# Optimization experiments

Measured on AMD Instinct MI355X. Metric: run time of the kernel, lower is better.

## Reference

```python
import jax, jax.numpy as jnp
import numpy as np

N, IN_DIM, H1, H2, LIN, MAX_INDEX = 16384, 64, 256, 256, 64, 256


def _init_layer(key, out_dim, in_dim):
    # mimic kaiming_uniform(a=sqrt(5)) + uniform bias bound = 1/sqrt(fan_in)
    kW, kb = jax.random.split(key)
    bound_w = 1.0 / np.sqrt(in_dim)  # gain*sqrt(3/fan_in) with a=sqrt(5) -> 1/sqrt(fan_in)
    W = jax.random.uniform(kW, (MAX_INDEX, out_dim, in_dim), jnp.float32, -bound_w, bound_w)
    b = jax.random.uniform(kb, (MAX_INDEX, out_dim), jnp.float32, -bound_w, bound_w)
    return W, b


def setup_inputs() -> dict:
    key = jax.random.key(0)
    kx, ki, k1, k2, k3 = jax.random.split(key, 5)
    x = jax.random.normal(kx, (N, IN_DIM), jnp.float32)
    ind = jax.random.randint(ki, (N,), 0, MAX_INDEX, jnp.int64 if jax.config.jax_enable_x64 else jnp.int32)
    W1, b1 = _init_layer(k1, H1, IN_DIM)
    W2, b2 = _init_layer(k2, H2, H1)
    Wl, bl = _init_layer(k3, LIN, H2)
    return {"x": x, "ind": ind, "W1": W1, "b1": b1, "W2": W2, "b2": b2, "Wl": Wl, "bl": bl}


def _index_linear(x, ind, W, b):
    # per-row expert weight gather then row-wise matvec: out[n] = W[ind[n]] @ x[n] + b[ind[n]]
    return jnp.einsum('noi,ni->no', W[ind], x) + b[ind]


def reference(x, ind, W1, b1, W2, b2, Wl, bl):
    h = jnp.tanh(_index_linear(x, ind, W1, b1))
    h = jnp.tanh(_index_linear(h, ind, W2, b2))
    return _index_linear(h, ind, Wl, bl)
```

## Files before the change

kernel.cpp:

```cpp
#include <hip/hip_runtime.h>
#include <hip/hip_bf16.h>
#include <math.h>

#define NROWS   16384
#define IN_DIM  64
#define HID     256
#define OUT_DIM 64
#define NEXP    256
#define MT      32
#define HP      264

typedef __attribute__((ext_vector_type(8))) short short8;
typedef __attribute__((ext_vector_type(4))) float f32x4;
typedef __attribute__((ext_vector_type(4))) unsigned uint4v;
typedef __attribute__((ext_vector_type(2))) unsigned uint2v;


__global__ __launch_bounds__(1024) void prep_k(const int* __restrict__ ind,
                                               int* __restrict__ rows,
                                               int* __restrict__ offsets) {
  __shared__ int hist[NEXP];
  __shared__ int scan[NEXP];
  __shared__ int cur[NEXP];
  int t = threadIdx.x;
  if (t < NEXP) hist[t] = 0;
  __syncthreads();
  for (int n = t; n < NROWS; n += 1024) atomicAdd(&hist[ind[n]], 1);
  __syncthreads();
  if (t < NEXP) scan[t] = hist[t];
  __syncthreads();
  for (int d = 1; d < NEXP; d <<= 1) {
    int v = (t < NEXP && t >= d) ? scan[t - d] : 0;
    __syncthreads();
    if (t < NEXP) scan[t] += v;
    __syncthreads();
  }
  if (t < NEXP) {
    int exc = scan[t] - hist[t];
    offsets[t] = exc;
    cur[t] = exc;
    if (t == NEXP - 1) offsets[NEXP] = scan[t];
  }
  __syncthreads();
  for (int n = t; n < NROWS; n += 1024) {
    int p = atomicAdd(&cur[ind[n]], 1);
    rows[p] = n;
  }
}


__device__ __forceinline__ unsigned pk2_trunc(float a, float b) {
  unsigned ua = __builtin_bit_cast(unsigned, a);
  unsigned ub = __builtin_bit_cast(unsigned, b);
  return (ub & 0xffff0000u) | (ua >> 16);
}

__device__ __forceinline__ unsigned pk2_rn(float a, float b) {
  __hip_bfloat162 h = __float22bfloat162_rn(float2{a, b});
  unsigned r;
  __builtin_memcpy(&r, &h, 4);
  return r;
}

__device__ __forceinline__ short8 cvt8w(f32x4 w0, f32x4 w1) {
  uint4v u;
  u.x = pk2_trunc(w0.x, w0.y);
  u.y = pk2_trunc(w0.z, w0.w);
  u.z = pk2_trunc(w1.x, w1.y);
  u.w = pk2_trunc(w1.z, w1.w);
  return __builtin_bit_cast(short8, u);
}

__device__ __forceinline__ float fast_tanh(float v) {
  float e = __expf(2.f * v);
  return 1.f - 2.f * __builtin_amdgcn_rcpf(e + 1.f);
}

template <int K, int NMT, int NNT>
__device__ __forceinline__ void layer_mm(const float* __restrict__ Wp,
                                         const float* __restrict__ bp,
                                         const unsigned short* Hin,
                                         int l15, int q, f32x4 (&acc)[NMT][NNT]) {
#pragma unroll
  for (int mt = 0; mt < NMT; mt++) {
    f32x4 bv = *(const f32x4*)(bp + mt * 16 + q * 4);
#pragma unroll
    for (int nt = 0; nt < NNT; nt++) acc[mt][nt] = bv;
  }
  const float* wr[NMT];
#pragma unroll
  for (int mt = 0; mt < NMT; mt++)
    wr[mt] = Wp + (size_t)(mt * 16 + l15) * K + q * 8;

  constexpr int KS = K / 32;
  f32x4 wcur[NMT][2], wnxt[NMT][2];
#pragma unroll
  for (int mt = 0; mt < NMT; mt++) {
    wcur[mt][0] = *(const f32x4*)(wr[mt]);
    wcur[mt][1] = *(const f32x4*)(wr[mt] + 4);
  }
#pragma unroll
  for (int ks = 0; ks < KS; ks++) {
    int kn = (ks + 1 < KS) ? (ks + 1) * 32 : 0;
#pragma unroll
    for (int mt = 0; mt < NMT; mt++) {
      wnxt[mt][0] = *(const f32x4*)(wr[mt] + kn);
      wnxt[mt][1] = *(const f32x4*)(wr[mt] + kn + 4);
    }
    short8 bfr[NNT];
#pragma unroll
    for (int nt = 0; nt < NNT; nt++)
      bfr[nt] = *(const short8*)&Hin[(nt * 16 + l15) * HP + ks * 32 + q * 8];
#pragma unroll
    for (int mt = 0; mt < NMT; mt++) {
      short8 a = cvt8w(wcur[mt][0], wcur[mt][1]);
#pragma unroll
      for (int nt = 0; nt < NNT; nt++)
        acc[mt][nt] =
            __builtin_amdgcn_mfma_f32_16x16x32_bf16(a, bfr[nt], acc[mt][nt], 0, 0, 0);
    }
#pragma unroll
    for (int mt = 0; mt < NMT; mt++) {
      wcur[mt][0] = wnxt[mt][0];
      wcur[mt][1] = wnxt[mt][1];
    }
  }
}

template <int NNT>
__device__ __forceinline__ void write_h(f32x4 (&acc)[4][NNT], unsigned short* H,
                                        int w, int l15, int q) {
#pragma unroll
  for (int mt = 0; mt < 4; mt++)
#pragma unroll
    for (int nt = 0; nt < NNT; nt++) {
      uint2v v;
      v.x = pk2_rn(fast_tanh(acc[mt][nt].x), fast_tanh(acc[mt][nt].y));
      v.y = pk2_rn(fast_tanh(acc[mt][nt].z), fast_tanh(acc[mt][nt].w));
      *(uint2v*)&H[(nt * 16 + l15) * HP + w * 64 + mt * 16 + q * 4] = v;
    }
}


__global__ __launch_bounds__(256, 2) void mlp_k(
    const float* __restrict__ x,
    const float* __restrict__ W1, const float* __restrict__ b1,
    const float* __restrict__ W2, const float* __restrict__ b2,
    const float* __restrict__ Wl, const float* __restrict__ bl,
    const int* __restrict__ rows, const int* __restrict__ offsets,
    float* __restrict__ out) {
  __shared__ __align__(16) unsigned short H[MT * HP];

  const int t = threadIdx.x;
  const int w = t >> 6;
  const int l15 = t & 15;
  const int q = (t >> 4) & 3;
  const int e = blockIdx.x & 255;
  const int j = blockIdx.x >> 8;
  const int beg = offsets[e];
  const int cnt = offsets[e + 1] - beg;

  const float* W1e = W1 + (size_t)e * HID * IN_DIM + (size_t)(w * 64) * IN_DIM;
  const float* W2e = W2 + (size_t)e * HID * HID + (size_t)(w * 64) * HID;
  const float* Wle = Wl + (size_t)e * OUT_DIM * HID + (size_t)(w * 16) * HID;
  const float* b1e = b1 + e * HID + w * 64;
  const float* b2e = b2 + e * HID + w * 64;
  const float* ble = bl + e * OUT_DIM + w * 16;

  const int sm = t >> 3;
  const int sc = (t & 7) * 8;

  for (int mt0 = j * MT; mt0 < cnt; mt0 += 2 * MT) {
    __syncthreads();
    {
      int gm = mt0 + sm;
      bool val = gm < cnt;
      int r = val ? rows[beg + gm] : 0;
      const float* xr = x + (size_t)r * IN_DIM + sc;
      uint4v u;
      if (val) {
        f32x4 a0 = *(const f32x4*)(xr);
        f32x4 a1 = *(const f32x4*)(xr + 4);
        u.x = pk2_rn(a0.x, a0.y); u.y = pk2_rn(a0.z, a0.w);
        u.z = pk2_rn(a1.x, a1.y); u.w = pk2_rn(a1.z, a1.w);
      } else {
        u = (uint4v){0, 0, 0, 0};
      }
      *(uint4v*)&H[sm * HP + sc] = u;
    }
    __syncthreads();

    {
      f32x4 acc[4][2];
      layer_mm<IN_DIM, 4, 2>(W1e, b1e, H, l15, q, acc);
      __syncthreads();
      write_h<2>(acc, H, w, l15, q);
    }
    __syncthreads();

    {
      f32x4 acc[4][2];
      layer_mm<HID, 4, 2>(W2e, b2e, H, l15, q, acc);
      __syncthreads();
      write_h<2>(acc, H, w, l15, q);
    }
    __syncthreads();

    {
      f32x4 acc[1][2];
      layer_mm<HID, 1, 2>(Wle, ble, H, l15, q, acc);
#pragma unroll
      for (int nt = 0; nt < 2; nt++) {
        int gm = mt0 + nt * 16 + l15;
        if (gm < cnt) {
          int r = rows[beg + gm];
          *(f32x4*)(out + (size_t)r * OUT_DIM + w * 16 + q * 4) = acc[0][nt];
        }
      }
    }
  }
}


extern "C" void kernel_launch(void* const* d_in, const int* in_sizes, int n_in,
                              void* d_out, int out_size, void* d_ws, size_t ws_size,
                              hipStream_t stream) {
  const float* x   = (const float*)d_in[0];
  const int*   ind = (const int*)d_in[1];
  const float* W1  = (const float*)d_in[2];
  const float* b1  = (const float*)d_in[3];
  const float* W2  = (const float*)d_in[4];
  const float* b2  = (const float*)d_in[5];
  const float* Wl  = (const float*)d_in[6];
  const float* bl  = (const float*)d_in[7];
  float* out = (float*)d_out;

  int* offsets = (int*)d_ws;
  int* rows    = (int*)d_ws + 260;

  prep_k<<<1, 1024, 0, stream>>>(ind, rows, offsets);
  mlp_k<<<NEXP * 2, 256, 0, stream>>>(x, W1, b1, W2, b2, Wl, bl, rows, offsets, out);
}
```

Measured before the change: 187.3 us.

## Use one 1024-thread block per expert with larger row tiles

Measured after the change: 171.1 us. 1.1x faster.

```diff
diff --git a/kernel.cpp b/kernel.cpp
--- a/kernel.cpp
+++ b/kernel.cpp
@@ -7,7 +7,7 @@
 #define HID     256
 #define OUT_DIM 64
 #define NEXP    256
-#define MT      32
+#define MT      112
 #define HP      264
 
 typedef __attribute__((ext_vector_type(8))) short short8;
@@ -76,73 +76,50 @@
   return 1.f - 2.f * __builtin_amdgcn_rcpf(e + 1.f);
 }
 
-template <int K, int NMT, int NNT>
-__device__ __forceinline__ void layer_mm(const float* __restrict__ Wp,
-                                         const float* __restrict__ bp,
-                                         const unsigned short* Hin,
-                                         int l15, int q, f32x4 (&acc)[NMT][NNT]) {
-#pragma unroll
-  for (int mt = 0; mt < NMT; mt++) {
-    f32x4 bv = *(const f32x4*)(bp + mt * 16 + q * 4);
-#pragma unroll
-    for (int nt = 0; nt < NNT; nt++) acc[mt][nt] = bv;
-  }
-  const float* wr[NMT];
-#pragma unroll
-  for (int mt = 0; mt < NMT; mt++)
-    wr[mt] = Wp + (size_t)(mt * 16 + l15) * K + q * 8;
-
+template <int K, int NNT>
+__device__ __forceinline__ void layer_mm1(const float* __restrict__ wr,
+                                          f32x4 bv,
+                                          const unsigned short* __restrict__ Hin,
+                                          int l15, int q, f32x4 (&acc)[NNT]) {
   constexpr int KS = K / 32;
-  f32x4 wcur[NMT][2], wnxt[NMT][2];
-#pragma unroll
-  for (int mt = 0; mt < NMT; mt++) {
-    wcur[mt][0] = *(const f32x4*)(wr[mt]);
-    wcur[mt][1] = *(const f32x4*)(wr[mt] + 4);
+#pragma unroll
+  for (int nt = 0; nt < NNT; nt++) acc[nt] = bv;
+  f32x4 wbuf[3][2];
+  wbuf[0][0] = *(const f32x4*)(wr);
+  wbuf[0][1] = *(const f32x4*)(wr + 4);
+  if (KS > 1) {
+    wbuf[1][0] = *(const f32x4*)(wr + 32);
+    wbuf[1][1] = *(const f32x4*)(wr + 36);
   }
 #pragma unroll
   for (int ks = 0; ks < KS; ks++) {
-    int kn = (ks + 1 < KS) ? (ks + 1) * 32 : 0;
-#pragma unroll
-    for (int mt = 0; mt < NMT; mt++) {
-      wnxt[mt][0] = *(const f32x4*)(wr[mt] + kn);
-      wnxt[mt][1] = *(const f32x4*)(wr[mt] + kn + 4);
-    }
-    short8 bfr[NNT];
-#pragma unroll
-    for (int nt = 0; nt < NNT; nt++)
-      bfr[nt] = *(const short8*)&Hin[(nt * 16 + l15) * HP + ks * 32 + q * 8];
-#pragma unroll
-    for (int mt = 0; mt < NMT; mt++) {
-      short8 a = cvt8w(wcur[mt][0], wcur[mt][1]);
-#pragma unroll
-      for (int nt = 0; nt < NNT; nt++)
-        acc[mt][nt] =
-            __builtin_amdgcn_mfma_f32_16x16x32_bf16(a, bfr[nt], acc[mt][nt], 0, 0, 0);
-    }
-#pragma unroll
-    for (int mt = 0; mt < NMT; mt++) {
-      wcur[mt][0] = wnxt[mt][0];
-      wcur[mt][1] = wnxt[mt][1];
+    if (ks + 2 < KS) {
+      wbuf[(ks + 2) % 3][0] = *(const f32x4*)(wr + (ks + 2) * 32);
+      wbuf[(ks + 2) % 3][1] = *(const f32x4*)(wr + (ks + 2) * 32 + 4);
+    }
+    short8 a = cvt8w(wbuf[ks % 3][0], wbuf[ks % 3][1]);
+#pragma unroll
+    for (int nt = 0; nt < NNT; nt++) {
+      short8 b = *(const short8*)&Hin[(nt * 16 + l15) * HP + ks * 32 + q * 8];
+      acc[nt] = __builtin_amdgcn_mfma_f32_16x16x32_bf16(a, b, acc[nt], 0, 0, 0);
     }
   }
 }
 
 template <int NNT>
-__device__ __forceinline__ void write_h(f32x4 (&acc)[4][NNT], unsigned short* H,
-                                        int w, int l15, int q) {
-#pragma unroll
-  for (int mt = 0; mt < 4; mt++)
-#pragma unroll
-    for (int nt = 0; nt < NNT; nt++) {
-      uint2v v;
-      v.x = pk2_rn(fast_tanh(acc[mt][nt].x), fast_tanh(acc[mt][nt].y));
-      v.y = pk2_rn(fast_tanh(acc[mt][nt].z), fast_tanh(acc[mt][nt].w));
-      *(uint2v*)&H[(nt * 16 + l15) * HP + w * 64 + mt * 16 + q * 4] = v;
-    }
-}
-
-
-__global__ __launch_bounds__(256, 2) void mlp_k(
+__device__ __forceinline__ void write_h1(f32x4 (&acc)[NNT], unsigned short* H,
+                                         int col, int l15) {
+#pragma unroll
+  for (int nt = 0; nt < NNT; nt++) {
+    uint2v v;
+    v.x = pk2_rn(fast_tanh(acc[nt].x), fast_tanh(acc[nt].y));
+    v.y = pk2_rn(fast_tanh(acc[nt].z), fast_tanh(acc[nt].w));
+    *(uint2v*)&H[(nt * 16 + l15) * HP + col] = v;
+  }
+}
+
+
+__global__ __launch_bounds__(1024, 4) void mlp_k(
     const float* __restrict__ x,
     const float* __restrict__ W1, const float* __restrict__ b1,
     const float* __restrict__ W2, const float* __restrict__ b2,
@@ -155,24 +132,26 @@
   const int w = t >> 6;
   const int l15 = t & 15;
   const int q = (t >> 4) & 3;
-  const int e = blockIdx.x & 255;
-  const int j = blockIdx.x >> 8;
+  const int e = blockIdx.x;
   const int beg = offsets[e];
   const int cnt = offsets[e + 1] - beg;
 
-  const float* W1e = W1 + (size_t)e * HID * IN_DIM + (size_t)(w * 64) * IN_DIM;
-  const float* W2e = W2 + (size_t)e * HID * HID + (size_t)(w * 64) * HID;
-  const float* Wle = Wl + (size_t)e * OUT_DIM * HID + (size_t)(w * 16) * HID;
-  const float* b1e = b1 + e * HID + w * 64;
-  const float* b2e = b2 + e * HID + w * 64;
-  const float* ble = bl + e * OUT_DIM + w * 16;
+  const float* W1e = W1 + (size_t)e * HID * IN_DIM + (size_t)(w * 16 + l15) * IN_DIM + q * 8;
+  const float* W2e = W2 + (size_t)e * HID * HID + (size_t)(w * 16 + l15) * HID + q * 8;
+  const int m3 = w & 3;
+  const int ntA = w >> 2;
+  const int nt1 = (ntA + 4 < 7) ? ntA + 4 : 6;
+  const float* Wle = Wl + (size_t)e * OUT_DIM * HID + (size_t)(m3 * 16 + l15) * HID + q * 8;
+  const f32x4 b1v = *(const f32x4*)(b1 + e * HID + w * 16 + q * 4);
+  const f32x4 b2v = *(const f32x4*)(b2 + e * HID + w * 16 + q * 4);
+  const f32x4 blv = *(const f32x4*)(bl + e * OUT_DIM + m3 * 16 + q * 4);
 
   const int sm = t >> 3;
   const int sc = (t & 7) * 8;
 
-  for (int mt0 = j * MT; mt0 < cnt; mt0 += 2 * MT) {
-    __syncthreads();
-    {
+  for (int mt0 = 0; mt0 < cnt; mt0 += MT) {
+    if (mt0) __syncthreads();
+    if (sm < MT) {
       int gm = mt0 + sm;
       bool val = gm < cnt;
       int r = val ? rows[beg + gm] : 0;
@@ -191,30 +170,53 @@
     __syncthreads();
 
     {
-      f32x4 acc[4][2];
-      layer_mm<IN_DIM, 4, 2>(W1e, b1e, H, l15, q, acc);
+      f32x4 acc[7];
+      layer_mm1<IN_DIM, 7>(W1e, b1v, H, l15, q, acc);
       __syncthreads();
-      write_h<2>(acc, H, w, l15, q);
+      write_h1<7>(acc, H, w * 16 + q * 4, l15);
     }
     __syncthreads();
 
     {
-      f32x4 acc[4][2];
-      layer_mm<HID, 4, 2>(W2e, b2e, H, l15, q, acc);
+      f32x4 acc[7];
+      layer_mm1<HID, 7>(W2e, b2v, H, l15, q, acc);
       __syncthreads();
-      write_h<2>(acc, H, w, l15, q);
+      write_h1<7>(acc, H, w * 16 + q * 4, l15);
     }
     __syncthreads();
 
     {
-      f32x4 acc[1][2];
-      layer_mm<HID, 1, 2>(Wle, ble, H, l15, q, acc);
-#pragma unroll
-      for (int nt = 0; nt < 2; nt++) {
-        int gm = mt0 + nt * 16 + l15;
+      f32x4 acc[2];
+      acc[0] = blv; acc[1] = blv;
+      f32x4 wbuf[3][2];
+      wbuf[0][0] = *(const f32x4*)(Wle);
+      wbuf[0][1] = *(const f32x4*)(Wle + 4);
+      wbuf[1][0] = *(const f32x4*)(Wle + 32);
+      wbuf[1][1] = *(const f32x4*)(Wle + 36);
+#pragma unroll
+      for (int ks = 0; ks < 8; ks++) {
+        if (ks + 2 < 8) {
+          wbuf[(ks + 2) % 3][0] = *(const f32x4*)(Wle + (ks + 2) * 32);
+          wbuf[(ks + 2) % 3][1] = *(const f32x4*)(Wle + (ks + 2) * 32 + 4);
+        }
+        short8 a = cvt8w(wbuf[ks % 3][0], wbuf[ks % 3][1]);
+        short8 bA = *(const short8*)&H[(ntA * 16 + l15) * HP + ks * 32 + q * 8];
+        short8 bB = *(const short8*)&H[(nt1 * 16 + l15) * HP + ks * 32 + q * 8];
+        acc[0] = __builtin_amdgcn_mfma_f32_16x16x32_bf16(a, bA, acc[0], 0, 0, 0);
+        acc[1] = __builtin_amdgcn_mfma_f32_16x16x32_bf16(a, bB, acc[1], 0, 0, 0);
+      }
+      {
+        int gm = mt0 + ntA * 16 + l15;
         if (gm < cnt) {
           int r = rows[beg + gm];
-          *(f32x4*)(out + (size_t)r * OUT_DIM + w * 16 + q * 4) = acc[0][nt];
+          *(f32x4*)(out + (size_t)r * OUT_DIM + m3 * 16 + q * 4) = acc[0];
+        }
+      }
+      if (ntA + 4 < 7) {
+        int gm = mt0 + nt1 * 16 + l15;
+        if (gm < cnt) {
+          int r = rows[beg + gm];
+          *(f32x4*)(out + (size_t)r * OUT_DIM + m3 * 16 + q * 4) = acc[1];
         }
       }
     }
@@ -239,5 +241,5 @@
   int* rows    = (int*)d_ws + 260;
 
   prep_k<<<1, 1024, 0, stream>>>(ind, rows, offsets);
-  mlp_k<<<NEXP * 2, 256, 0, stream>>>(x, W1, b1, W2, b2, Wl, bl, rows, offsets, out);
-}
+  mlp_k<<<NEXP, 1024, 0, stream>>>(x, W1, b1, W2, b2, Wl, bl, rows, offsets, out);
+}
```
